# Kernel optimization log

Hardware: AMD Instinct MI355X
Metric: run time of the kernel (lower is better)

## Reference

```python
import jax, jax.numpy as jnp
import numpy as np


def setup_inputs() -> dict:
    key = jax.random.key(0)
    k1, k2, k3, k4 = jax.random.split(key, 4)
    b, l, v, s = 2, 2048, 8, 64
    return {
        "query": jax.random.normal(k1, (b, l, v, s), dtype=jnp.float32),
        "key": jax.random.normal(k2, (b, l, v, s), dtype=jnp.float32),
        "value": jax.random.normal(k3, (b, l, v, s), dtype=jnp.float32),
        "label_arr": jax.random.randint(k4, (b, l), 0, 8, dtype=jnp.int64),
    }


def reference(query, key, value, label_arr):
    # query/key/value: (b, l, v, s); label_arr computed into a mask in the
    # original code but never applied, so it does not affect the math.
    b, l, v, s = query.shape
    scale = 1.0 / np.sqrt(s).astype(np.float32)
    # key summed over the v (head) axis -> pooled key per token: (b, l, s)
    sum_tot_vec = key.sum(axis=2)
    # scores[b,l,v,m] = <query[b,l,v,:], sum_tot_vec[b,m,:]>  (the torch per-v loop, batched)
    scores = jnp.einsum("blvs,bms->blvm", query, sum_tot_vec)
    A = jax.nn.softmax(scale * scores, axis=-1)  # (b, l, v, l)
    # V[b,l,v,s] = sum_m A[b,l,v,m] * value[b,m,v,s]  (the broadcast-multiply+sum, as a matmul)
    V = jnp.einsum("blvm,bmvs->blvs", A, value)
    return V
```

## Files before the change

### kernel.cpp

```cpp
#include <hip/hip_runtime.h>


#define BB 2
#define LL 2048
#define HH 8
#define DD 64

typedef __attribute__((ext_vector_type(8)))  short  short8;
typedef __attribute__((ext_vector_type(16))) float  float16v;

static __device__ inline unsigned short f2bf(float x) {
    union { float f; unsigned u; } v; v.f = x;
    unsigned r = v.u + 0x7FFF + ((v.u >> 16) & 1);
    return (unsigned short)(r >> 16);
}
static __device__ inline unsigned pk_bf2(float x, float y) {
    return (unsigned)f2bf(x) | ((unsigned)f2bf(y) << 16);
}

__global__ __launch_bounds__(256)
void prep_kernel(const float* __restrict__ key, const float* __restrict__ value,
                 unsigned short* __restrict__ kswz,
                 unsigned short* __restrict__ vswz) {
    __shared__ __align__(16) float Vl[64][68];
    int bid = blockIdx.x;
    int tid = threadIdx.x;

    if (bid < 512) {
        int mt = bid & 31, bh = bid >> 5;
        int h = bh & 7, b = bh >> 3;
        int m0 = mt * 64;
#pragma unroll
        for (int k = 0; k < 4; ++k) {
            int f = tid + k * 256;
            int r = f >> 4;
            int cc = (f & 15) * 4;
            float4 t = *(const float4*)(value +
                (((size_t)(b * LL + m0 + r)) * HH + h) * DD + cc);
            *(float4*)&Vl[r][cc] = t;
        }
        __syncthreads();
#pragma unroll
        for (int k = 0; k < 2; ++k) {
            int c    = tid + k * 256;
            int Tl   = c >> 8;
            int t    = (c >> 7) & 1;
            int vh   = (c >> 6) & 1;
            int lane = c & 63;
            int ln = lane & 31, half = lane >> 5;
            union { short8 v; unsigned short u[8]; } o;
#pragma unroll
            for (int jj = 0; jj < 8; ++jj) {
                int r2 = t * 8 + jj;
                int m  = (r2 & 3) + 8 * (r2 >> 2) + 4 * half;
                o.u[jj] = f2bf(Vl[Tl * 32 + m][vh * 32 + ln]);
            }
            *(short8*)(vswz +
                ((((size_t)bh * 64 + (mt * 2 + Tl)) * 4 + t * 2 + vh) * 512)
                + lane * 8) = o.v;
        }
    } else {
        const float LOG2E = 1.4426950408889634f;
        int pb    = bid - 512;
        int chunk = pb * 4 + (tid >> 6);
        int lane  = tid & 63;
        int b = chunk >> 8, T = (chunk >> 2) & 63, ks = chunk & 3;
        int ln = lane & 31, hf = lane >> 5;
        const float* base = key + (((size_t)(b * LL + T * 32 + ln)) * HH) * DD
                                + ks * 16 + hf * 8;
        float s[8];
#pragma unroll
        for (int j = 0; j < 8; ++j) s[j] = 0.f;
#pragma unroll
        for (int v = 0; v < HH; ++v) {
            float4 f0 = *(const float4*)(base + v * DD);
            float4 f1 = *(const float4*)(base + v * DD + 4);
            s[0] += f0.x; s[1] += f0.y; s[2] += f0.z; s[3] += f0.w;
            s[4] += f1.x; s[5] += f1.y; s[6] += f1.z; s[7] += f1.w;
        }
        union { short8 v; unsigned u[4]; } o;
#pragma unroll
        for (int i = 0; i < 4; ++i)
            o.u[i] = pk_bf2(s[2 * i] * LOG2E, s[2 * i + 1] * LOG2E);
        *(short8*)(kswz + (size_t)chunk * 512 + lane * 8) = o.v;
    }
}

__global__ __launch_bounds__(256, 3)
void attn_kernel(const float* __restrict__ query,
                 const unsigned short* __restrict__ kswz,
                 const unsigned short* __restrict__ vswz,
                 float* __restrict__ out) {
    int bid = blockIdx.x;
    int bh  = bid & 15;
    int qt  = bid >> 4;
    int h = bh & 7, b = bh >> 3;

    int tid  = threadIdx.x;
    int lane = tid & 63;
    int wv   = tid >> 6;
    int ln   = lane & 31;
    int half = lane >> 5;

    __shared__ float O2[2][64][68];
    __shared__ float lsumL[4][128];
    __shared__ float invL[64];

    short8 qf[2][4];
#pragma unroll
    for (int g = 0; g < 2; ++g) {
        const float* qbase = query +
            (((size_t)(b * LL + qt * 64 + g * 32 + ln)) * HH + h) * DD;
#pragma unroll
        for (int ks = 0; ks < 4; ++ks) {
            const float4* qp = (const float4*)(qbase + ks * 16 + half * 8);
            float4 t0 = qp[0], t1 = qp[1];
            union { short8 v; unsigned u[4]; } uq;
            uq.u[0] = pk_bf2(t0.x * 0.125f, t0.y * 0.125f);
            uq.u[1] = pk_bf2(t0.z * 0.125f, t0.w * 0.125f);
            uq.u[2] = pk_bf2(t1.x * 0.125f, t1.y * 0.125f);
            uq.u[3] = pk_bf2(t1.z * 0.125f, t1.w * 0.125f);
            qf[g][ks] = uq.v;
        }
    }

    const unsigned short* kp0 = kswz + (((size_t)b * 64 + wv * 16) * 4) * 512
                                     + (size_t)lane * 8;
    const unsigned short* vp0 = vswz + (((size_t)bh * 64 + wv * 16) * 4) * 512
                                     + (size_t)lane * 8;

    float16v o00, o01, o10, o11;
#pragma unroll
    for (int i = 0; i < 16; ++i) { o00[i] = 0.f; o01[i] = 0.f; o10[i] = 0.f; o11[i] = 0.f; }
    float ls0a = 0.f, ls0b = 0.f, ls1a = 0.f, ls1b = 0.f;

#pragma unroll
    for (int it = 0; it < 16; ++it) {
        short8 kf[4], vf[4];
#pragma unroll
        for (int ks = 0; ks < 4; ++ks)
            kf[ks] = *(const short8*)(kp0 + it * 2048 + ks * 512);
#pragma unroll
        for (int u = 0; u < 4; ++u)
            vf[u] = *(const short8*)(vp0 + it * 2048 + u * 512);

#pragma unroll
        for (int g = 0; g < 2; ++g) {
            float16v sacc;
#pragma unroll
            for (int i = 0; i < 16; ++i) sacc[i] = 0.f;
#pragma unroll
            for (int ks = 0; ks < 4; ++ks)
                sacc = __builtin_amdgcn_mfma_f32_32x32x16_bf16(kf[ks], qf[g][ks], sacc, 0, 0, 0);

            union { short8 v[2]; unsigned u[8]; } pu;
#pragma unroll
            for (int i = 0; i < 8; ++i) {
                union { float f; unsigned u; } e0, e1;
                e0.f = exp2f(sacc[2 * i]);
                e1.f = exp2f(sacc[2 * i + 1]);
                if (g == 0) { ls0a += e0.f; ls0b += e1.f; }
                else        { ls1a += e0.f; ls1b += e1.f; }
                pu.u[i] = __builtin_amdgcn_perm(e1.u + 0x8000u, e0.u + 0x8000u, 0x07060302u);
            }

            if (g == 0) {
                o00 = __builtin_amdgcn_mfma_f32_32x32x16_bf16(pu.v[0], vf[0], o00, 0, 0, 0);
                o01 = __builtin_amdgcn_mfma_f32_32x32x16_bf16(pu.v[0], vf[1], o01, 0, 0, 0);
                o00 = __builtin_amdgcn_mfma_f32_32x32x16_bf16(pu.v[1], vf[2], o00, 0, 0, 0);
                o01 = __builtin_amdgcn_mfma_f32_32x32x16_bf16(pu.v[1], vf[3], o01, 0, 0, 0);
            } else {
                o10 = __builtin_amdgcn_mfma_f32_32x32x16_bf16(pu.v[0], vf[0], o10, 0, 0, 0);
                o11 = __builtin_amdgcn_mfma_f32_32x32x16_bf16(pu.v[0], vf[1], o11, 0, 0, 0);
                o10 = __builtin_amdgcn_mfma_f32_32x32x16_bf16(pu.v[1], vf[2], o10, 0, 0, 0);
                o11 = __builtin_amdgcn_mfma_f32_32x32x16_bf16(pu.v[1], vf[3], o11, 0, 0, 0);
            }
        }
    }

    lsumL[wv][lane]      = ls0a + ls0b;
    lsumL[wv][64 + lane] = ls1a + ls1b;
    if (wv < 2) {
#pragma unroll
        for (int r = 0; r < 16; ++r) {
            int row = (r & 3) + 8 * (r >> 2) + 4 * half;
            O2[wv][row][ln]           = o00[r];
            O2[wv][row][32 + ln]      = o01[r];
            O2[wv][32 + row][ln]      = o10[r];
            O2[wv][32 + row][32 + ln] = o11[r];
        }
    }
    __syncthreads();
    if (wv >= 2) {
#pragma unroll
        for (int r = 0; r < 16; ++r) {
            int row = (r & 3) + 8 * (r >> 2) + 4 * half;
            O2[wv - 2][row][ln]           += o00[r];
            O2[wv - 2][row][32 + ln]      += o01[r];
            O2[wv - 2][32 + row][ln]      += o10[r];
            O2[wv - 2][32 + row][32 + ln] += o11[r];
        }
    }
    __syncthreads();

    if (tid < 64) {
        int g = tid >> 5, c = tid & 31;
        float s = 0.f;
#pragma unroll
        for (int w = 0; w < 4; ++w)
            s += lsumL[w][g * 64 + c] + lsumL[w][g * 64 + 32 + c];
        invL[tid] = 1.0f / s;
    }
    __syncthreads();

    int qrow = tid >> 2;
    int c16  = (tid & 3) * 16;
    float inv = invL[qrow];
    float buf[16];
#pragma unroll
    for (int j = 0; j < 16; ++j)
        buf[j] = (O2[0][qrow][c16 + j] + O2[1][qrow][c16 + j]) * inv;
    float* ob = out + (((size_t)(b * LL + qt * 64 + qrow)) * HH + h) * DD + c16;
#pragma unroll
    for (int j = 0; j < 4; ++j)
        *(float4*)(ob + 4 * j) = make_float4(buf[4 * j], buf[4 * j + 1],
                                             buf[4 * j + 2], buf[4 * j + 3]);
}

extern "C" void kernel_launch(void* const* d_in, const int* in_sizes, int n_in,
                              void* d_out, int out_size, void* d_ws, size_t ws_size,
                              hipStream_t stream) {
    const float* query = (const float*)d_in[0];
    const float* key   = (const float*)d_in[1];
    const float* value = (const float*)d_in[2];
    float* out = (float*)d_out;

    unsigned short* kswz = (unsigned short*)d_ws;
    unsigned short* vswz = (unsigned short*)((char*)d_ws + 512 * 1024);

    prep_kernel<<<640, 256, 0, stream>>>(key, value, kswz, vswz);
    attn_kernel<<<512, 256, 0, stream>>>(query, kswz, vswz, out);
}
```

Baseline: 107.2 us.

## Halve query tile per block, split keys across eight waves, prefetch K/V

Each block now processes 32 query rows with 512 threads, and the key range is split across eight waves instead of four with two query groups each. Next-iteration K/V fragments are loaded ahead of the exp/PV work to overlap memory latency. This is meant to cut registers per wave and add parallelism and occupancy. In exchange, K/V loads are reused by only one query group, so global/L2 traffic doubles and the cross-wave LDS reduction grows.

```diff
diff --git a/kernel.cpp b/kernel.cpp
--- a/kernel.cpp
+++ b/kernel.cpp
@@ -86,7 +86,7 @@
     }
 }
 
-__global__ __launch_bounds__(256, 3)
+__global__ __launch_bounds__(512, 4)
 void attn_kernel(const float* __restrict__ query,
                  const unsigned short* __restrict__ kswz,
                  const unsigned short* __restrict__ vswz,
@@ -102,129 +102,119 @@
     int ln   = lane & 31;
     int half = lane >> 5;
 
-    __shared__ float O2[2][64][68];
-    __shared__ float lsumL[4][128];
-    __shared__ float invL[64];
-
-    short8 qf[2][4];
-#pragma unroll
-    for (int g = 0; g < 2; ++g) {
-        const float* qbase = query +
-            (((size_t)(b * LL + qt * 64 + g * 32 + ln)) * HH + h) * DD;
-#pragma unroll
-        for (int ks = 0; ks < 4; ++ks) {
-            const float4* qp = (const float4*)(qbase + ks * 16 + half * 8);
-            float4 t0 = qp[0], t1 = qp[1];
-            union { short8 v; unsigned u[4]; } uq;
-            uq.u[0] = pk_bf2(t0.x * 0.125f, t0.y * 0.125f);
-            uq.u[1] = pk_bf2(t0.z * 0.125f, t0.w * 0.125f);
-            uq.u[2] = pk_bf2(t1.x * 0.125f, t1.y * 0.125f);
-            uq.u[3] = pk_bf2(t1.z * 0.125f, t1.w * 0.125f);
-            qf[g][ks] = uq.v;
-        }
-    }
-
-    const unsigned short* kp0 = kswz + (((size_t)b * 64 + wv * 16) * 4) * 512
+    __shared__ float O4[4][32][DD];
+    __shared__ float lsumL[8][64];
+    __shared__ float invL[32];
+
+    short8 qf[4];
+    const float* qbase = query + (((size_t)(b * LL + qt * 32 + ln)) * HH + h) * DD;
+#pragma unroll
+    for (int ks = 0; ks < 4; ++ks) {
+        const float4* qp = (const float4*)(qbase + ks * 16 + half * 8);
+        float4 t0 = qp[0], t1 = qp[1];
+        union { short8 v; unsigned u[4]; } uq;
+        uq.u[0] = pk_bf2(t0.x * 0.125f, t0.y * 0.125f);
+        uq.u[1] = pk_bf2(t0.z * 0.125f, t0.w * 0.125f);
+        uq.u[2] = pk_bf2(t1.x * 0.125f, t1.y * 0.125f);
+        uq.u[3] = pk_bf2(t1.z * 0.125f, t1.w * 0.125f);
+        qf[ks] = uq.v;
+    }
+
+    const unsigned short* kp0 = kswz + (((size_t)b * 64 + wv * 8) * 4) * 512
                                      + (size_t)lane * 8;
-    const unsigned short* vp0 = vswz + (((size_t)bh * 64 + wv * 16) * 4) * 512
+    const unsigned short* vp0 = vswz + (((size_t)bh * 64 + wv * 8) * 4) * 512
                                      + (size_t)lane * 8;
 
-    float16v o00, o01, o10, o11;
-#pragma unroll
-    for (int i = 0; i < 16; ++i) { o00[i] = 0.f; o01[i] = 0.f; o10[i] = 0.f; o11[i] = 0.f; }
-    float ls0a = 0.f, ls0b = 0.f, ls1a = 0.f, ls1b = 0.f;
-
-#pragma unroll
-    for (int it = 0; it < 16; ++it) {
-        short8 kf[4], vf[4];
+    float16v o0, o1;
+#pragma unroll
+    for (int i = 0; i < 16; ++i) { o0[i] = 0.f; o1[i] = 0.f; }
+    float lsa = 0.f, lsb = 0.f;
+
+    short8 kf[4], vf[4];
+#pragma unroll
+    for (int ks = 0; ks < 4; ++ks) kf[ks] = *(const short8*)(kp0 + ks * 512);
+#pragma unroll
+    for (int u = 0; u < 4; ++u)    vf[u]  = *(const short8*)(vp0 + u * 512);
+
+#pragma unroll
+    for (int it = 0; it < 8; ++it) {
+        float16v sacc;
+#pragma unroll
+        for (int i = 0; i < 16; ++i) sacc[i] = 0.f;
 #pragma unroll
         for (int ks = 0; ks < 4; ++ks)
-            kf[ks] = *(const short8*)(kp0 + it * 2048 + ks * 512);
-#pragma unroll
-        for (int u = 0; u < 4; ++u)
-            vf[u] = *(const short8*)(vp0 + it * 2048 + u * 512);
-
-#pragma unroll
-        for (int g = 0; g < 2; ++g) {
-            float16v sacc;
-#pragma unroll
-            for (int i = 0; i < 16; ++i) sacc[i] = 0.f;
+            sacc = __builtin_amdgcn_mfma_f32_32x32x16_bf16(kf[ks], qf[ks], sacc, 0, 0, 0);
+
+        short8 kn[4], vn[4];
+        if (it + 1 < 8) {
 #pragma unroll
             for (int ks = 0; ks < 4; ++ks)
-                sacc = __builtin_amdgcn_mfma_f32_32x32x16_bf16(kf[ks], qf[g][ks], sacc, 0, 0, 0);
-
-            union { short8 v[2]; unsigned u[8]; } pu;
-#pragma unroll
-            for (int i = 0; i < 8; ++i) {
-                union { float f; unsigned u; } e0, e1;
-                e0.f = exp2f(sacc[2 * i]);
-                e1.f = exp2f(sacc[2 * i + 1]);
-                if (g == 0) { ls0a += e0.f; ls0b += e1.f; }
-                else        { ls1a += e0.f; ls1b += e1.f; }
-                pu.u[i] = __builtin_amdgcn_perm(e1.u + 0x8000u, e0.u + 0x8000u, 0x07060302u);
-            }
-
-            if (g == 0) {
-                o00 = __builtin_amdgcn_mfma_f32_32x32x16_bf16(pu.v[0], vf[0], o00, 0, 0, 0);
-                o01 = __builtin_amdgcn_mfma_f32_32x32x16_bf16(pu.v[0], vf[1], o01, 0, 0, 0);
-                o00 = __builtin_amdgcn_mfma_f32_32x32x16_bf16(pu.v[1], vf[2], o00, 0, 0, 0);
-                o01 = __builtin_amdgcn_mfma_f32_32x32x16_bf16(pu.v[1], vf[3], o01, 0, 0, 0);
-            } else {
-                o10 = __builtin_amdgcn_mfma_f32_32x32x16_bf16(pu.v[0], vf[0], o10, 0, 0, 0);
-                o11 = __builtin_amdgcn_mfma_f32_32x32x16_bf16(pu.v[0], vf[1], o11, 0, 0, 0);
-                o10 = __builtin_amdgcn_mfma_f32_32x32x16_bf16(pu.v[1], vf[2], o10, 0, 0, 0);
-                o11 = __builtin_amdgcn_mfma_f32_32x32x16_bf16(pu.v[1], vf[3], o11, 0, 0, 0);
-            }
-        }
-    }
-
-    lsumL[wv][lane]      = ls0a + ls0b;
-    lsumL[wv][64 + lane] = ls1a + ls1b;
-    if (wv < 2) {
+                kn[ks] = *(const short8*)(kp0 + (it + 1) * 2048 + ks * 512);
+#pragma unroll
+            for (int u = 0; u < 4; ++u)
+                vn[u]  = *(const short8*)(vp0 + (it + 1) * 2048 + u * 512);
+        }
+
+        union { short8 v[2]; unsigned u[8]; } pu;
+#pragma unroll
+        for (int i = 0; i < 8; ++i) {
+            union { float f; unsigned u; } e0, e1;
+            e0.f = exp2f(sacc[2 * i]);
+            e1.f = exp2f(sacc[2 * i + 1]);
+            lsa += e0.f; lsb += e1.f;
+            pu.u[i] = __builtin_amdgcn_perm(e1.u + 0x8000u, e0.u + 0x8000u, 0x07060302u);
+        }
+
+        o0 = __builtin_amdgcn_mfma_f32_32x32x16_bf16(pu.v[0], vf[0], o0, 0, 0, 0);
+        o1 = __builtin_amdgcn_mfma_f32_32x32x16_bf16(pu.v[0], vf[1], o1, 0, 0, 0);
+        o0 = __builtin_amdgcn_mfma_f32_32x32x16_bf16(pu.v[1], vf[2], o0, 0, 0, 0);
+        o1 = __builtin_amdgcn_mfma_f32_32x32x16_bf16(pu.v[1], vf[3], o1, 0, 0, 0);
+
+        if (it + 1 < 8) {
+#pragma unroll
+            for (int ks = 0; ks < 4; ++ks) kf[ks] = kn[ks];
+#pragma unroll
+            for (int u = 0; u < 4; ++u)    vf[u]  = vn[u];
+        }
+    }
+
+    lsumL[wv][lane] = lsa + lsb;
+    if (wv < 4) {
 #pragma unroll
         for (int r = 0; r < 16; ++r) {
             int row = (r & 3) + 8 * (r >> 2) + 4 * half;
-            O2[wv][row][ln]           = o00[r];
-            O2[wv][row][32 + ln]      = o01[r];
-            O2[wv][32 + row][ln]      = o10[r];
-            O2[wv][32 + row][32 + ln] = o11[r];
+            O4[wv][row][ln]      = o0[r];
+            O4[wv][row][32 + ln] = o1[r];
         }
     }
     __syncthreads();
-    if (wv >= 2) {
+    if (wv >= 4) {
 #pragma unroll
         for (int r = 0; r < 16; ++r) {
             int row = (r & 3) + 8 * (r >> 2) + 4 * half;
-            O2[wv - 2][row][ln]           += o00[r];
-            O2[wv - 2][row][32 + ln]      += o01[r];
-            O2[wv - 2][32 + row][ln]      += o10[r];
-            O2[wv - 2][32 + row][32 + ln] += o11[r];
+            O4[wv - 4][row][ln]      += o0[r];
+            O4[wv - 4][row][32 + ln] += o1[r];
         }
     }
     __syncthreads();
 
-    if (tid < 64) {
-        int g = tid >> 5, c = tid & 31;
+    if (tid < 32) {
         float s = 0.f;
 #pragma unroll
-        for (int w = 0; w < 4; ++w)
-            s += lsumL[w][g * 64 + c] + lsumL[w][g * 64 + 32 + c];
+        for (int w = 0; w < 8; ++w) s += lsumL[w][tid] + lsumL[w][tid + 32];
         invL[tid] = 1.0f / s;
     }
     __syncthreads();
 
-    int qrow = tid >> 2;
-    int c16  = (tid & 3) * 16;
+    int qrow = tid >> 4;
+    int c4   = (tid & 15) * 4;
     float inv = invL[qrow];
-    float buf[16];
-#pragma unroll
-    for (int j = 0; j < 16; ++j)
-        buf[j] = (O2[0][qrow][c16 + j] + O2[1][qrow][c16 + j]) * inv;
-    float* ob = out + (((size_t)(b * LL + qt * 64 + qrow)) * HH + h) * DD + c16;
-#pragma unroll
-    for (int j = 0; j < 4; ++j)
-        *(float4*)(ob + 4 * j) = make_float4(buf[4 * j], buf[4 * j + 1],
-                                             buf[4 * j + 2], buf[4 * j + 3]);
+    float4 r;
+    r.x = (O4[0][qrow][c4 + 0] + O4[1][qrow][c4 + 0] + O4[2][qrow][c4 + 0] + O4[3][qrow][c4 + 0]) * inv;
+    r.y = (O4[0][qrow][c4 + 1] + O4[1][qrow][c4 + 1] + O4[2][qrow][c4 + 1] + O4[3][qrow][c4 + 1]) * inv;
+    r.z = (O4[0][qrow][c4 + 2] + O4[1][qrow][c4 + 2] + O4[2][qrow][c4 + 2] + O4[3][qrow][c4 + 2]) * inv;
+    r.w = (O4[0][qrow][c4 + 3] + O4[1][qrow][c4 + 3] + O4[2][qrow][c4 + 3] + O4[3][qrow][c4 + 3]) * inv;
+    *(float4*)(out + (((size_t)(b * LL + qt * 32 + qrow)) * HH + h) * DD + c4) = r;
 }
 
 extern "C" void kernel_launch(void* const* d_in, const int* in_sizes, int n_in,
@@ -239,5 +229,5 @@
     unsigned short* vswz = (unsigned short*)((char*)d_ws + 512 * 1024);
 
     prep_kernel<<<640, 256, 0, stream>>>(key, value, kswz, vswz);
-    attn_kernel<<<512, 256, 0, stream>>>(query, kswz, vswz, out);
-}
+    attn_kernel<<<1024, 512, 0, stream>>>(query, kswz, vswz, out);
+}
```

Result: slower. 173.9 us (+62.1%).

## Software-pipeline K/V fragment loads and interleave both query groups' MFMAs

Applied to the files above, without the earlier changes.

Hoists the first K and V fragment loads out of the loop and prefetches the next iteration's K and V fragments while the current iteration computes. It also interleaves the score MFMAs and PV MFMAs of the two query groups to expose more independent work. Occupancy is relaxed from 3 to 2 waves per SIMD to leave room for the extra live registers. The risk is that lower occupancy hides latency less well than the explicit prefetch does.

```diff
diff --git a/kernel.cpp b/kernel.cpp
--- a/kernel.cpp
+++ b/kernel.cpp
@@ -86,7 +86,7 @@
     }
 }
 
-__global__ __launch_bounds__(256, 3)
+__global__ __launch_bounds__(256, 2)
 void attn_kernel(const float* __restrict__ query,
                  const unsigned short* __restrict__ kswz,
                  const unsigned short* __restrict__ vswz,
@@ -134,47 +134,59 @@
     for (int i = 0; i < 16; ++i) { o00[i] = 0.f; o01[i] = 0.f; o10[i] = 0.f; o11[i] = 0.f; }
     float ls0a = 0.f, ls0b = 0.f, ls1a = 0.f, ls1b = 0.f;
 
+    short8 kf[4], vf[4];
+#pragma unroll
+    for (int ks = 0; ks < 4; ++ks) kf[ks] = *(const short8*)(kp0 + ks * 512);
+#pragma unroll
+    for (int u = 0; u < 4; ++u)    vf[u]  = *(const short8*)(vp0 + u * 512);
+
 #pragma unroll
     for (int it = 0; it < 16; ++it) {
-        short8 kf[4], vf[4];
-#pragma unroll
-        for (int ks = 0; ks < 4; ++ks)
-            kf[ks] = *(const short8*)(kp0 + it * 2048 + ks * 512);
-#pragma unroll
-        for (int u = 0; u < 4; ++u)
-            vf[u] = *(const short8*)(vp0 + it * 2048 + u * 512);
-
-#pragma unroll
-        for (int g = 0; g < 2; ++g) {
-            float16v sacc;
-#pragma unroll
-            for (int i = 0; i < 16; ++i) sacc[i] = 0.f;
+        float16v s0, s1;
+#pragma unroll
+        for (int i = 0; i < 16; ++i) { s0[i] = 0.f; s1[i] = 0.f; }
+#pragma unroll
+        for (int ks = 0; ks < 4; ++ks) {
+            s0 = __builtin_amdgcn_mfma_f32_32x32x16_bf16(kf[ks], qf[0][ks], s0, 0, 0, 0);
+            s1 = __builtin_amdgcn_mfma_f32_32x32x16_bf16(kf[ks], qf[1][ks], s1, 0, 0, 0);
+        }
+        if (it + 1 < 16) {
 #pragma unroll
             for (int ks = 0; ks < 4; ++ks)
-                sacc = __builtin_amdgcn_mfma_f32_32x32x16_bf16(kf[ks], qf[g][ks], sacc, 0, 0, 0);
-
-            union { short8 v[2]; unsigned u[8]; } pu;
-#pragma unroll
-            for (int i = 0; i < 8; ++i) {
-                union { float f; unsigned u; } e0, e1;
-                e0.f = exp2f(sacc[2 * i]);
-                e1.f = exp2f(sacc[2 * i + 1]);
-                if (g == 0) { ls0a += e0.f; ls0b += e1.f; }
-                else        { ls1a += e0.f; ls1b += e1.f; }
-                pu.u[i] = __builtin_amdgcn_perm(e1.u + 0x8000u, e0.u + 0x8000u, 0x07060302u);
-            }
-
-            if (g == 0) {
-                o00 = __builtin_amdgcn_mfma_f32_32x32x16_bf16(pu.v[0], vf[0], o00, 0, 0, 0);
-                o01 = __builtin_amdgcn_mfma_f32_32x32x16_bf16(pu.v[0], vf[1], o01, 0, 0, 0);
-                o00 = __builtin_amdgcn_mfma_f32_32x32x16_bf16(pu.v[1], vf[2], o00, 0, 0, 0);
-                o01 = __builtin_amdgcn_mfma_f32_32x32x16_bf16(pu.v[1], vf[3], o01, 0, 0, 0);
-            } else {
-                o10 = __builtin_amdgcn_mfma_f32_32x32x16_bf16(pu.v[0], vf[0], o10, 0, 0, 0);
-                o11 = __builtin_amdgcn_mfma_f32_32x32x16_bf16(pu.v[0], vf[1], o11, 0, 0, 0);
-                o10 = __builtin_amdgcn_mfma_f32_32x32x16_bf16(pu.v[1], vf[2], o10, 0, 0, 0);
-                o11 = __builtin_amdgcn_mfma_f32_32x32x16_bf16(pu.v[1], vf[3], o11, 0, 0, 0);
-            }
+                kf[ks] = *(const short8*)(kp0 + (it + 1) * 2048 + ks * 512);
+        }
+
+        union { short8 v[2]; unsigned u[8]; } pu0, pu1;
+#pragma unroll
+        for (int i = 0; i < 8; ++i) {
+            union { float f; unsigned u; } e0, e1;
+            e0.f = exp2f(s0[2 * i]);
+            e1.f = exp2f(s0[2 * i + 1]);
+            ls0a += e0.f; ls0b += e1.f;
+            pu0.u[i] = __builtin_amdgcn_perm(e1.u + 0x8000u, e0.u + 0x8000u, 0x07060302u);
+        }
+#pragma unroll
+        for (int i = 0; i < 8; ++i) {
+            union { float f; unsigned u; } e0, e1;
+            e0.f = exp2f(s1[2 * i]);
+            e1.f = exp2f(s1[2 * i + 1]);
+            ls1a += e0.f; ls1b += e1.f;
+            pu1.u[i] = __builtin_amdgcn_perm(e1.u + 0x8000u, e0.u + 0x8000u, 0x07060302u);
+        }
+
+        o00 = __builtin_amdgcn_mfma_f32_32x32x16_bf16(pu0.v[0], vf[0], o00, 0, 0, 0);
+        o01 = __builtin_amdgcn_mfma_f32_32x32x16_bf16(pu0.v[0], vf[1], o01, 0, 0, 0);
+        o10 = __builtin_amdgcn_mfma_f32_32x32x16_bf16(pu1.v[0], vf[0], o10, 0, 0, 0);
+        o11 = __builtin_amdgcn_mfma_f32_32x32x16_bf16(pu1.v[0], vf[1], o11, 0, 0, 0);
+        o00 = __builtin_amdgcn_mfma_f32_32x32x16_bf16(pu0.v[1], vf[2], o00, 0, 0, 0);
+        o01 = __builtin_amdgcn_mfma_f32_32x32x16_bf16(pu0.v[1], vf[3], o01, 0, 0, 0);
+        o10 = __builtin_amdgcn_mfma_f32_32x32x16_bf16(pu1.v[1], vf[2], o10, 0, 0, 0);
+        o11 = __builtin_amdgcn_mfma_f32_32x32x16_bf16(pu1.v[1], vf[3], o11, 0, 0, 0);
+
+        if (it + 1 < 16) {
+#pragma unroll
+            for (int u = 0; u < 4; ++u)
+                vf[u] = *(const short8*)(vp0 + (it + 1) * 2048 + u * 512);
         }
     }
 
```

After: 106.2 us. No clear change (-0.9%).
